# Kernel optimization log

Hardware: AMD Instinct MI355X
Metric: run time of the kernel (lower is better)

## Reference

```python
import jax, jax.numpy as jnp
import numpy as np

BLOCK_LEN = 64

def _segsum(x):
    """x: (..., T) -> (..., T, T) with segment sums on/below diagonal, -inf above."""
    T = x.shape[-1]
    cs = jnp.cumsum(x, axis=-1)
    seg = cs[..., :, None] - cs[..., None, :]
    mask = jnp.tril(jnp.ones((T, T), dtype=bool))
    return jnp.where(mask, seg, -jnp.inf)

def setup_inputs() -> dict:
    key = jax.random.key(0)
    kX, kA, kB, kC = jax.random.split(key, 4)
    B, S, H, P, N = 2, 4096, 32, 64, 64
    X = jax.random.normal(kX, (B, S, H, P), dtype=jnp.float32)
    # negative decay rates keep exp(cumsum) bounded (real Mamba2 uses A<0)
    A = -jnp.abs(jax.random.normal(kA, (B, S, H), dtype=jnp.float32)) * 0.1
    Bm = jax.random.normal(kB, (B, S, H, N), dtype=jnp.float32)
    Cm = jax.random.normal(kC, (B, S, H, N), dtype=jnp.float32)
    return {"X": X, "A": A, "Bm": Bm, "Cm": Cm}

def reference(X, A, Bm, Cm):
    b, s, h, p = X.shape
    n = Bm.shape[-1]
    l = BLOCK_LEN
    c = s // l
    Xb = X.reshape(b, c, l, h, p)
    Bb = Bm.reshape(b, c, l, h, n)
    Cb = Cm.reshape(b, c, l, h, n)
    Ab = A.reshape(b, c, l, h).transpose(0, 3, 1, 2)  # (b,h,c,l)

    # intra-chunk decay matrix L = exp(segsum(A))  (b,h,c,l,l)
    L = jnp.exp(_segsum(Ab))
    Y_diag = jnp.einsum('bclhn,bcshn,bhcls,bcshp->bclhp', Cb, Bb, L, Xb)

    A_cumsum = jnp.cumsum(Ab, axis=-1)  # (b,h,c,l)
    decay_states = jnp.exp(A_cumsum[..., :, -1:] - A_cumsum)
    states = jnp.einsum('bclhn,bhcl,bclhp->bchpn', Bb, decay_states, Xb)

    init = jnp.zeros_like(states[:, :1])
    states = jnp.concatenate([init, states], axis=1)  # (b,c+1,h,p,n)

    chunk_last = jnp.pad(A_cumsum[..., -1], ((0, 0), (0, 0), (1, 0)))  # (b,h,c+1)
    decay_chunk = jnp.exp(_segsum(chunk_last))  # (b,h,c+1,c+1)
    new_states = jnp.einsum('bhzc,bchpn->bzhpn', decay_chunk, states)
    states = new_states[:, :-1]  # (b,c,h,p,n)

    state_decay_out = jnp.exp(A_cumsum)
    Y_off = jnp.einsum('bclhn,bchpn,bhcl->bclhp', Cb, states, state_decay_out)

    Y = (Y_diag + Y_off).reshape(b, s, h, p)
    return Y
```

## Files before the change

kernel.cpp:

```cpp
#include <hip/hip_runtime.h>
#include <hip/hip_bf16.h>

#define B_ 2
#define S_ 4096
#define H_ 32
#define P_ 64
#define N_ 64
#define C_ 64
#define HP 2048
#define HN 2048

__device__ __forceinline__ float bf2f(unsigned int u16) {
    return __uint_as_float(u16 << 16);
}
__device__ __forceinline__ void unpack2(unsigned int u, float& lo, float& hi) {
    lo = __uint_as_float(u << 16);
    hi = __uint_as_float(u & 0xffff0000u);
}
__device__ __forceinline__ unsigned short f2bf(float f) {
    unsigned int u = __float_as_uint(f);
    u += 0x7fffu + ((u >> 16) & 1u);
    return (unsigned short)(u >> 16);
}

__global__ void k0_detect(const unsigned short* __restrict__ Au, int* __restrict__ flag)
{
    int tid = threadIdx.x;
    unsigned short u = Au[tid * 2];
    int positive = ((u & 0x8000u) == 0) ? 1 : 0;
    unsigned long long m = __ballot(positive);
    if (tid == 0) *flag = (__popcll(m) > 8) ? 1 : 0;
}

__global__ __launch_bounds__(256) void k1_states(
    const void* __restrict__ Xg,
    const void* __restrict__ Ag,
    const void* __restrict__ Bg,
    float* __restrict__ states,
    float* __restrict__ sums,
    const int* __restrict__ flag)
{
    __shared__ __align__(16) float Xs[64][68];
    __shared__ __align__(16) float BwT[64][68];
    __shared__ float wdec[64];

    const int tid = threadIdx.x;
    const int bid = blockIdx.x;
    const int h = bid & 31;
    const int c = (bid >> 5) & 63;
    const int b = bid >> 11;
    const int isf32 = *flag;

    if (tid < 64) {
        int ai = (b * S_ + c * 64 + tid) * H_ + h;
        float a = isf32 ? ((const float*)Ag)[ai] : bf2f(((const unsigned short*)Ag)[ai]);
        float x = a;
        #pragma unroll
        for (int off = 1; off < 64; off <<= 1) {
            float y = __shfl_up(x, off, 64);
            if (tid >= off) x += y;
        }
        float tot = __shfl(x, 63, 64);
        wdec[tid] = __expf(tot - x);
        if (tid == 63) sums[(b * H_ + h) * C_ + c] = tot;
    }
    __syncthreads();

    const size_t baseX = (size_t)((b * S_ + c * 64) * H_ + h) * P_;
    const size_t baseB = (size_t)((b * S_ + c * 64) * H_ + h) * N_;

    if (!isf32) {
        const unsigned short* Xp = (const unsigned short*)Xg + baseX;
        const unsigned short* Bp = (const unsigned short*)Bg + baseB;
        #pragma unroll
        for (int it = 0; it < 2; ++it) {
            int f = it * 2048 + tid * 8;
            int t = f >> 6;
            int e = f & 63;
            uint4 rx = *(const uint4*)(Xp + (size_t)t * HP + e);
            float v0,v1,v2,v3,v4,v5,v6,v7;
            unpack2(rx.x, v0, v1); unpack2(rx.y, v2, v3);
            unpack2(rx.z, v4, v5); unpack2(rx.w, v6, v7);
            float* xr = &Xs[t][e];
            xr[0]=v0; xr[1]=v1; xr[2]=v2; xr[3]=v3; xr[4]=v4; xr[5]=v5; xr[6]=v6; xr[7]=v7;

            uint4 rb = *(const uint4*)(Bp + (size_t)t * HN + e);
            float w = wdec[t];
            unpack2(rb.x, v0, v1); unpack2(rb.y, v2, v3);
            unpack2(rb.z, v4, v5); unpack2(rb.w, v6, v7);
            BwT[e+0][t]=v0*w; BwT[e+1][t]=v1*w; BwT[e+2][t]=v2*w; BwT[e+3][t]=v3*w;
            BwT[e+4][t]=v4*w; BwT[e+5][t]=v5*w; BwT[e+6][t]=v6*w; BwT[e+7][t]=v7*w;
        }
    } else {
        const float* Xp = (const float*)Xg + baseX;
        const float* Bp = (const float*)Bg + baseB;
        #pragma unroll
        for (int it = 0; it < 2; ++it) {
            int f = it * 2048 + tid * 8;
            int t = f >> 6;
            int e = f & 63;
            float4 x0 = *(const float4*)(Xp + (size_t)t * HP + e);
            float4 x1 = *(const float4*)(Xp + (size_t)t * HP + e + 4);
            float* xr = &Xs[t][e];
            xr[0]=x0.x; xr[1]=x0.y; xr[2]=x0.z; xr[3]=x0.w;
            xr[4]=x1.x; xr[5]=x1.y; xr[6]=x1.z; xr[7]=x1.w;

            float4 b0 = *(const float4*)(Bp + (size_t)t * HN + e);
            float4 b1 = *(const float4*)(Bp + (size_t)t * HN + e + 4);
            float w = wdec[t];
            BwT[e+0][t]=b0.x*w; BwT[e+1][t]=b0.y*w; BwT[e+2][t]=b0.z*w; BwT[e+3][t]=b0.w*w;
            BwT[e+4][t]=b1.x*w; BwT[e+5][t]=b1.y*w; BwT[e+6][t]=b1.z*w; BwT[e+7][t]=b1.w*w;
        }
    }
    __syncthreads();

    const int tr = tid >> 4, tc = tid & 15;
    float acc[4][4];
    #pragma unroll
    for (int i = 0; i < 4; ++i)
        #pragma unroll
        for (int j = 0; j < 4; ++j) acc[i][j] = 0.f;

    #pragma unroll 4
    for (int k4 = 0; k4 < 16; ++k4) {
        float la[4][4];
        #pragma unroll
        for (int i = 0; i < 4; ++i) {
            float4 v = *(const float4*)&BwT[tr * 4 + i][k4 * 4];
            la[i][0]=v.x; la[i][1]=v.y; la[i][2]=v.z; la[i][3]=v.w;
        }
        #pragma unroll
        for (int kk = 0; kk < 4; ++kk) {
            float4 r = *(const float4*)&Xs[k4 * 4 + kk][tc * 4];
            #pragma unroll
            for (int i = 0; i < 4; ++i) {
                acc[i][0] += la[i][kk] * r.x;
                acc[i][1] += la[i][kk] * r.y;
                acc[i][2] += la[i][kk] * r.z;
                acc[i][3] += la[i][kk] * r.w;
            }
        }
    }

    float* sp = states + (size_t)((b * C_ + c) * H_ + h) * 4096;
    #pragma unroll
    for (int i = 0; i < 4; ++i) {
        float4 v; v.x=acc[i][0]; v.y=acc[i][1]; v.z=acc[i][2]; v.w=acc[i][3];
        *(float4*)&sp[(tr * 4 + i) * 64 + tc * 4] = v;
    }
}

__global__ __launch_bounds__(256) void k2_scan(
    float* __restrict__ states, const float* __restrict__ sums)
{
    const int tid = threadIdx.x;
    const int bid = blockIdx.x;
    const int split = bid & 3;
    const int bh = bid >> 2;
    const int h = bh & 31;
    const int b = bh >> 5;
    const int e = split * 1024 + tid * 4;
    const float* sm = sums + (b * H_ + h) * C_;
    float4 S; S.x=0.f; S.y=0.f; S.z=0.f; S.w=0.f;
    for (int c = 0; c < 64; ++c) {
        float* p = states + (size_t)((b * C_ + c) * H_ + h) * 4096 + e;
        float4 st = *(const float4*)p;
        *(float4*)p = S;
        float d = __expf(sm[c]);
        S.x = S.x * d + st.x;
        S.y = S.y * d + st.y;
        S.z = S.z * d + st.z;
        S.w = S.w * d + st.w;
    }
}

__global__ __launch_bounds__(256) void k3_y(
    const void* __restrict__ Xg,
    const void* __restrict__ Ag,
    const void* __restrict__ Bg,
    const void* __restrict__ Cg,
    const float* __restrict__ states,
    void* __restrict__ Yg,
    const int* __restrict__ flag)
{
    __shared__ __align__(16) float Cs[64][68];
    __shared__ __align__(16) float Mb[64][68];
    __shared__ __align__(16) float Rb[64][68];
    __shared__ float cs[64];

    const int tid = threadIdx.x;
    const int bid = blockIdx.x;
    const int h = bid & 31;
    const int c = (bid >> 5) & 63;
    const int b = bid >> 11;
    const int isf32 = *flag;

    if (tid < 64) {
        int ai = (b * S_ + c * 64 + tid) * H_ + h;
        float a = isf32 ? ((const float*)Ag)[ai] : bf2f(((const unsigned short*)Ag)[ai]);
        float x = a;
        #pragma unroll
        for (int off = 1; off < 64; off <<= 1) {
            float y = __shfl_up(x, off, 64);
            if (tid >= off) x += y;
        }
        cs[tid] = x;
    }

    const size_t baseX = (size_t)((b * S_ + c * 64) * H_ + h) * P_;
    const size_t baseN = (size_t)((b * S_ + c * 64) * H_ + h) * N_;

    if (!isf32) {
        const unsigned short* Bp = (const unsigned short*)Bg + baseN;
        const unsigned short* Cp = (const unsigned short*)Cg + baseN;
        #pragma unroll
        for (int it = 0; it < 2; ++it) {
            int f = it * 2048 + tid * 8;
            int t = f >> 6;
            int e = f & 63;
            uint4 rc = *(const uint4*)(Cp + (size_t)t * HN + e);
            float v0,v1,v2,v3,v4,v5,v6,v7;
            unpack2(rc.x, v0, v1); unpack2(rc.y, v2, v3);
            unpack2(rc.z, v4, v5); unpack2(rc.w, v6, v7);
            float* cr = &Cs[t][e];
            cr[0]=v0; cr[1]=v1; cr[2]=v2; cr[3]=v3; cr[4]=v4; cr[5]=v5; cr[6]=v6; cr[7]=v7;

            uint4 rb = *(const uint4*)(Bp + (size_t)t * HN + e);
            unpack2(rb.x, v0, v1); unpack2(rb.y, v2, v3);
            unpack2(rb.z, v4, v5); unpack2(rb.w, v6, v7);
            Rb[e+0][t]=v0; Rb[e+1][t]=v1; Rb[e+2][t]=v2; Rb[e+3][t]=v3;
            Rb[e+4][t]=v4; Rb[e+5][t]=v5; Rb[e+6][t]=v6; Rb[e+7][t]=v7;
        }
    } else {
        const float* Bp = (const float*)Bg + baseN;
        const float* Cp = (const float*)Cg + baseN;
        #pragma unroll
        for (int it = 0; it < 2; ++it) {
            int f = it * 2048 + tid * 8;
            int t = f >> 6;
            int e = f & 63;
            float4 c0 = *(const float4*)(Cp + (size_t)t * HN + e);
            float4 c1 = *(const float4*)(Cp + (size_t)t * HN + e + 4);
            float* cr = &Cs[t][e];
            cr[0]=c0.x; cr[1]=c0.y; cr[2]=c0.z; cr[3]=c0.w;
            cr[4]=c1.x; cr[5]=c1.y; cr[6]=c1.z; cr[7]=c1.w;

            float4 b0 = *(const float4*)(Bp + (size_t)t * HN + e);
            float4 b1 = *(const float4*)(Bp + (size_t)t * HN + e + 4);
            Rb[e+0][t]=b0.x; Rb[e+1][t]=b0.y; Rb[e+2][t]=b0.z; Rb[e+3][t]=b0.w;
            Rb[e+4][t]=b1.x; Rb[e+5][t]=b1.y; Rb[e+6][t]=b1.z; Rb[e+7][t]=b1.w;
        }
    }
    __syncthreads();

    const int tr = tid >> 4, tc = tid & 15;

    {
        float acc[4][4];
        #pragma unroll
        for (int i = 0; i < 4; ++i)
            #pragma unroll
            for (int j = 0; j < 4; ++j) acc[i][j] = 0.f;

        #pragma unroll 4
        for (int k4 = 0; k4 < 16; ++k4) {
            float la[4][4];
            #pragma unroll
            for (int i = 0; i < 4; ++i) {
                float4 v = *(const float4*)&Cs[tr * 4 + i][k4 * 4];
                la[i][0]=v.x; la[i][1]=v.y; la[i][2]=v.z; la[i][3]=v.w;
            }
            #pragma unroll
            for (int kk = 0; kk < 4; ++kk) {
                float4 r = *(const float4*)&Rb[k4 * 4 + kk][tc * 4];
                #pragma unroll
                for (int i = 0; i < 4; ++i) {
                    acc[i][0] += la[i][kk] * r.x;
                    acc[i][1] += la[i][kk] * r.y;
                    acc[i][2] += la[i][kk] * r.z;
                    acc[i][3] += la[i][kk] * r.w;
                }
            }
        }

        float ct[4], csj[4];
        #pragma unroll
        for (int i = 0; i < 4; ++i) ct[i] = cs[tr * 4 + i];
        #pragma unroll
        for (int j = 0; j < 4; ++j) csj[j] = cs[tc * 4 + j];
        #pragma unroll
        for (int i = 0; i < 4; ++i) {
            int t = tr * 4 + i;
            float4 mv;
            mv.x = (tc*4+0 <= t) ? acc[i][0] * __expf(ct[i]-csj[0]) : 0.f;
            mv.y = (tc*4+1 <= t) ? acc[i][1] * __expf(ct[i]-csj[1]) : 0.f;
            mv.z = (tc*4+2 <= t) ? acc[i][2] * __expf(ct[i]-csj[2]) : 0.f;
            mv.w = (tc*4+3 <= t) ? acc[i][3] * __expf(ct[i]-csj[3]) : 0.f;
            *(float4*)&Mb[t][tc * 4] = mv;
        }
    }
    __syncthreads();

    if (!isf32) {
        const unsigned short* Xp = (const unsigned short*)Xg + baseX;
        #pragma unroll
        for (int it = 0; it < 2; ++it) {
            int f = it * 2048 + tid * 8;
            int t = f >> 6;
            int e = f & 63;
            uint4 rx = *(const uint4*)(Xp + (size_t)t * HP + e);
            float v0,v1,v2,v3,v4,v5,v6,v7;
            unpack2(rx.x, v0, v1); unpack2(rx.y, v2, v3);
            unpack2(rx.z, v4, v5); unpack2(rx.w, v6, v7);
            float* xr = &Rb[t][e];
            xr[0]=v0; xr[1]=v1; xr[2]=v2; xr[3]=v3; xr[4]=v4; xr[5]=v5; xr[6]=v6; xr[7]=v7;
        }
    } else {
        const float* Xp = (const float*)Xg + baseX;
        #pragma unroll
        for (int it = 0; it < 2; ++it) {
            int f = it * 2048 + tid * 8;
            int t = f >> 6;
            int e = f & 63;
            float4 x0 = *(const float4*)(Xp + (size_t)t * HP + e);
            float4 x1 = *(const float4*)(Xp + (size_t)t * HP + e + 4);
            float* xr = &Rb[t][e];
            xr[0]=x0.x; xr[1]=x0.y; xr[2]=x0.z; xr[3]=x0.w;
            xr[4]=x1.x; xr[5]=x1.y; xr[6]=x1.z; xr[7]=x1.w;
        }
    }
    __syncthreads();

    float accD[4][4];
    #pragma unroll
    for (int i = 0; i < 4; ++i)
        #pragma unroll
        for (int j = 0; j < 4; ++j) accD[i][j] = 0.f;

    #pragma unroll 4
    for (int k4 = 0; k4 < 16; ++k4) {
        float la[4][4];
        #pragma unroll
        for (int i = 0; i < 4; ++i) {
            float4 v = *(const float4*)&Mb[tr * 4 + i][k4 * 4];
            la[i][0]=v.x; la[i][1]=v.y; la[i][2]=v.z; la[i][3]=v.w;
        }
        #pragma unroll
        for (int kk = 0; kk < 4; ++kk) {
            float4 r = *(const float4*)&Rb[k4 * 4 + kk][tc * 4];
            #pragma unroll
            for (int i = 0; i < 4; ++i) {
                accD[i][0] += la[i][kk] * r.x;
                accD[i][1] += la[i][kk] * r.y;
                accD[i][2] += la[i][kk] * r.z;
                accD[i][3] += la[i][kk] * r.w;
            }
        }
    }
    __syncthreads();

    {
        const float* sb = states + (size_t)((b * C_ + c) * H_ + h) * 4096;
        #pragma unroll
        for (int k = 0; k < 4; ++k) {
            int e2 = (k * 256 + tid) * 4;
            float4 v = *(const float4*)(sb + e2);
            *(float4*)&Rb[e2 >> 6][e2 & 63] = v;
        }
    }
    __syncthreads();

    float accO[4][4];
    #pragma unroll
    for (int i = 0; i < 4; ++i)
        #pragma unroll
        for (int j = 0; j < 4; ++j) accO[i][j] = 0.f;

    #pragma unroll 4
    for (int k4 = 0; k4 < 16; ++k4) {
        float la[4][4];
        #pragma unroll
        for (int i = 0; i < 4; ++i) {
            float4 v = *(const float4*)&Cs[tr * 4 + i][k4 * 4];
            la[i][0]=v.x; la[i][1]=v.y; la[i][2]=v.z; la[i][3]=v.w;
        }
        #pragma unroll
        for (int kk = 0; kk < 4; ++kk) {
            float4 r = *(const float4*)&Rb[k4 * 4 + kk][tc * 4];
            #pragma unroll
            for (int i = 0; i < 4; ++i) {
                accO[i][0] += la[i][kk] * r.x;
                accO[i][1] += la[i][kk] * r.y;
                accO[i][2] += la[i][kk] * r.z;
                accO[i][3] += la[i][kk] * r.w;
            }
        }
    }

    if (!isf32) {
        unsigned short* Yp = (unsigned short*)Yg + baseX;
        #pragma unroll
        for (int i = 0; i < 4; ++i) {
            int t = tr * 4 + i;
            float g = __expf(cs[t]);
            ushort4 o;
            o.x = f2bf(accD[i][0] + g * accO[i][0]);
            o.y = f2bf(accD[i][1] + g * accO[i][1]);
            o.z = f2bf(accD[i][2] + g * accO[i][2]);
            o.w = f2bf(accD[i][3] + g * accO[i][3]);
            *(ushort4*)(Yp + (size_t)t * HP + tc * 4) = o;
        }
    } else {
        float* Yp = (float*)Yg + baseX;
        #pragma unroll
        for (int i = 0; i < 4; ++i) {
            int t = tr * 4 + i;
            float g = __expf(cs[t]);
            float4 o;
            o.x = accD[i][0] + g * accO[i][0];
            o.y = accD[i][1] + g * accO[i][1];
            o.z = accD[i][2] + g * accO[i][2];
            o.w = accD[i][3] + g * accO[i][3];
            *(float4*)(Yp + (size_t)t * HP + tc * 4) = o;
        }
    }
}

extern "C" void kernel_launch(void* const* d_in, const int* in_sizes, int n_in,
                              void* d_out, int out_size, void* d_ws, size_t ws_size,
                              hipStream_t stream) {
    const void* X  = d_in[0];
    const void* A  = d_in[1];
    const void* Bm = d_in[2];
    const void* Cm = d_in[3];

    int*   flag   = (int*)d_ws;
    float* sums   = (float*)d_ws + 16;
    float* states = (float*)d_ws + 16 + 4096;

    k0_detect<<<dim3(1), dim3(64), 0, stream>>>((const unsigned short*)A, flag);
    k1_states<<<dim3(B_ * C_ * H_), dim3(256), 0, stream>>>(X, A, Bm, states, sums, flag);
    k2_scan  <<<dim3(B_ * H_ * 4),  dim3(256), 0, stream>>>(states, sums);
    k3_y     <<<dim3(B_ * C_ * H_), dim3(256), 0, stream>>>(X, A, Bm, Cm, states, d_out, flag);
}
```

Baseline: 334.1 us.

## Use split-bf16 MFMA matmuls in state and output kernels, widen scan split

Replaces the scalar FP32 shared-memory GEMMs in the chunk-state and output kernels with bf16 MFMA 16x16x32 instructions. Each fp32 operand is split into high and low bf16 parts and combined with three products, which keeps close to fp32 accuracy. Shared tiles move to swizzled bf16 layouts to avoid bank conflicts, and launch bounds are set to raise occupancy. The scan kernel is split eight ways with float2 accesses and a prefetch of the next chunk. The cost is extra split/convert work, more shared memory, and scalar (non-vector) global stores of the MFMA output layout.

Measured after the change: 282.6 us. -15.4%, faster.

```diff
diff --git a/kernel.cpp b/kernel.cpp
--- a/kernel.cpp
+++ b/kernel.cpp
@@ -1,5 +1,4 @@
 #include <hip/hip_runtime.h>
-#include <hip/hip_bf16.h>
 
 #define B_ 2
 #define S_ 4096
@@ -10,6 +9,9 @@
 #define HP 2048
 #define HN 2048
 
+typedef __attribute__((ext_vector_type(8))) short bf16x8;
+typedef __attribute__((ext_vector_type(4))) float f32x4;
+
 __device__ __forceinline__ float bf2f(unsigned int u16) {
     return __uint_as_float(u16 << 16);
 }
@@ -21,6 +23,17 @@
     unsigned int u = __float_as_uint(f);
     u += 0x7fffu + ((u >> 16) & 1u);
     return (unsigned short)(u >> 16);
+}
+__device__ __forceinline__ void split_bf(float x, unsigned short& h, unsigned short& l) {
+    h = f2bf(x);
+    l = f2bf(x - bf2f(h));
+}
+
+__device__ __forceinline__ int nsw(int r, int cb) {
+    return (r << 7) + (cb ^ ((r & 7) << 4));
+}
+__device__ __forceinline__ int tsw(int r, int cb) {
+    return (r << 7) + (cb ^ ((((r & 7) ^ (r >> 3)) & 7) << 4));
 }
 
 __global__ void k0_detect(const unsigned short* __restrict__ Au, int* __restrict__ flag)
@@ -32,7 +45,7 @@
     if (tid == 0) *flag = (__popcll(m) > 8) ? 1 : 0;
 }
 
-__global__ __launch_bounds__(256) void k1_states(
+__global__ __launch_bounds__(256, 4) void k1u(
     const void* __restrict__ Xg,
     const void* __restrict__ Ag,
     const void* __restrict__ Bg,
@@ -40,15 +53,15 @@
     float* __restrict__ sums,
     const int* __restrict__ flag)
 {
-    __shared__ __align__(16) float Xs[64][68];
-    __shared__ __align__(16) float BwT[64][68];
+    __shared__ __align__(16) unsigned short XTh[4096];
+    __shared__ __align__(16) unsigned short XTl[4096];
+    __shared__ __align__(16) unsigned short BTh[4096];
+    __shared__ __align__(16) unsigned short BTl[4096];
     __shared__ float wdec[64];
 
     const int tid = threadIdx.x;
     const int bid = blockIdx.x;
-    const int h = bid & 31;
-    const int c = (bid >> 5) & 63;
-    const int b = bid >> 11;
+    const int h = bid & 31, c = (bid >> 5) & 63, b = bid >> 11;
     const int isf32 = *flag;
 
     if (tid < 64) {
@@ -68,86 +81,91 @@
 
     const size_t baseX = (size_t)((b * S_ + c * 64) * H_ + h) * P_;
     const size_t baseB = (size_t)((b * S_ + c * 64) * H_ + h) * N_;
-
-    if (!isf32) {
-        const unsigned short* Xp = (const unsigned short*)Xg + baseX;
-        const unsigned short* Bp = (const unsigned short*)Bg + baseB;
-        #pragma unroll
-        for (int it = 0; it < 2; ++it) {
-            int f = it * 2048 + tid * 8;
-            int t = f >> 6;
-            int e = f & 63;
-            uint4 rx = *(const uint4*)(Xp + (size_t)t * HP + e);
-            float v0,v1,v2,v3,v4,v5,v6,v7;
-            unpack2(rx.x, v0, v1); unpack2(rx.y, v2, v3);
-            unpack2(rx.z, v4, v5); unpack2(rx.w, v6, v7);
-            float* xr = &Xs[t][e];
-            xr[0]=v0; xr[1]=v1; xr[2]=v2; xr[3]=v3; xr[4]=v4; xr[5]=v5; xr[6]=v6; xr[7]=v7;
-
-            uint4 rb = *(const uint4*)(Bp + (size_t)t * HN + e);
-            float w = wdec[t];
-            unpack2(rb.x, v0, v1); unpack2(rb.y, v2, v3);
-            unpack2(rb.z, v4, v5); unpack2(rb.w, v6, v7);
-            BwT[e+0][t]=v0*w; BwT[e+1][t]=v1*w; BwT[e+2][t]=v2*w; BwT[e+3][t]=v3*w;
-            BwT[e+4][t]=v4*w; BwT[e+5][t]=v5*w; BwT[e+6][t]=v6*w; BwT[e+7][t]=v7*w;
-        }
-    } else {
-        const float* Xp = (const float*)Xg + baseX;
-        const float* Bp = (const float*)Bg + baseB;
-        #pragma unroll
-        for (int it = 0; it < 2; ++it) {
-            int f = it * 2048 + tid * 8;
-            int t = f >> 6;
-            int e = f & 63;
-            float4 x0 = *(const float4*)(Xp + (size_t)t * HP + e);
-            float4 x1 = *(const float4*)(Xp + (size_t)t * HP + e + 4);
-            float* xr = &Xs[t][e];
-            xr[0]=x0.x; xr[1]=x0.y; xr[2]=x0.z; xr[3]=x0.w;
-            xr[4]=x1.x; xr[5]=x1.y; xr[6]=x1.z; xr[7]=x1.w;
-
-            float4 b0 = *(const float4*)(Bp + (size_t)t * HN + e);
-            float4 b1 = *(const float4*)(Bp + (size_t)t * HN + e + 4);
-            float w = wdec[t];
-            BwT[e+0][t]=b0.x*w; BwT[e+1][t]=b0.y*w; BwT[e+2][t]=b0.z*w; BwT[e+3][t]=b0.w*w;
-            BwT[e+4][t]=b1.x*w; BwT[e+5][t]=b1.y*w; BwT[e+6][t]=b1.z*w; BwT[e+7][t]=b1.w*w;
+    char* XThb = (char*)XTh;
+    char* XTlb = (char*)XTl;
+    char* BThb = (char*)BTh;
+    char* BTlb = (char*)BTl;
+
+    #pragma unroll
+    for (int it = 0; it < 2; ++it) {
+        int t = (tid >> 3) + it * 32;
+        int e = (tid & 7) * 8;
+        float xv[8], bv[8];
+        if (isf32) {
+            const float* Xp = (const float*)Xg + baseX + (size_t)t * HP + e;
+            const float* Bp = (const float*)Bg + baseB + (size_t)t * HN + e;
+            float4 x0 = *(const float4*)Xp;
+            float4 x1 = *(const float4*)(Xp + 4);
+            float4 b0 = *(const float4*)Bp;
+            float4 b1 = *(const float4*)(Bp + 4);
+            xv[0]=x0.x; xv[1]=x0.y; xv[2]=x0.z; xv[3]=x0.w;
+            xv[4]=x1.x; xv[5]=x1.y; xv[6]=x1.z; xv[7]=x1.w;
+            bv[0]=b0.x; bv[1]=b0.y; bv[2]=b0.z; bv[3]=b0.w;
+            bv[4]=b1.x; bv[5]=b1.y; bv[6]=b1.z; bv[7]=b1.w;
+        } else {
+            const unsigned short* Xp = (const unsigned short*)Xg + baseX + (size_t)t * HP + e;
+            const unsigned short* Bp = (const unsigned short*)Bg + baseB + (size_t)t * HN + e;
+            uint4 rx = *(const uint4*)Xp;
+            uint4 rb = *(const uint4*)Bp;
+            unpack2(rx.x, xv[0], xv[1]); unpack2(rx.y, xv[2], xv[3]);
+            unpack2(rx.z, xv[4], xv[5]); unpack2(rx.w, xv[6], xv[7]);
+            unpack2(rb.x, bv[0], bv[1]); unpack2(rb.y, bv[2], bv[3]);
+            unpack2(rb.z, bv[4], bv[5]); unpack2(rb.w, bv[6], bv[7]);
+        }
+        float w = wdec[t];
+        #pragma unroll
+        for (int i = 0; i < 8; ++i) {
+            int o = tsw(e + i, 2 * t);
+            unsigned short hh, ll;
+            split_bf(xv[i], hh, ll);
+            *(unsigned short*)(XThb + o) = hh;
+            *(unsigned short*)(XTlb + o) = ll;
+            split_bf(bv[i] * w, hh, ll);
+            *(unsigned short*)(BThb + o) = hh;
+            *(unsigned short*)(BTlb + o) = ll;
         }
     }
     __syncthreads();
 
-    const int tr = tid >> 4, tc = tid & 15;
-    float acc[4][4];
-    #pragma unroll
-    for (int i = 0; i < 4; ++i)
-        #pragma unroll
-        for (int j = 0; j < 4; ++j) acc[i][j] = 0.f;
-
-    #pragma unroll 4
-    for (int k4 = 0; k4 < 16; ++k4) {
-        float la[4][4];
-        #pragma unroll
-        for (int i = 0; i < 4; ++i) {
-            float4 v = *(const float4*)&BwT[tr * 4 + i][k4 * 4];
-            la[i][0]=v.x; la[i][1]=v.y; la[i][2]=v.z; la[i][3]=v.w;
-        }
-        #pragma unroll
-        for (int kk = 0; kk < 4; ++kk) {
-            float4 r = *(const float4*)&Xs[k4 * 4 + kk][tc * 4];
-            #pragma unroll
-            for (int i = 0; i < 4; ++i) {
-                acc[i][0] += la[i][kk] * r.x;
-                acc[i][1] += la[i][kk] * r.y;
-                acc[i][2] += la[i][kk] * r.z;
-                acc[i][3] += la[i][kk] * r.w;
-            }
-        }
+    const int l = tid & 63, w4 = tid >> 6;
+    const int lr = l & 15, q = l >> 4;
+    const int rowA = 16 * w4 + lr;
+
+    const int oa0 = tsw(rowA, 16 * q);
+    const int oa1 = tsw(rowA, 16 * q + 64);
+    bf16x8 a0h = *(const bf16x8*)(XThb + oa0);
+    bf16x8 a1h = *(const bf16x8*)(XThb + oa1);
+    bf16x8 a0l = *(const bf16x8*)(XTlb + oa0);
+    bf16x8 a1l = *(const bf16x8*)(XTlb + oa1);
+
+    f32x4 acc[4];
+    #pragma unroll
+    for (int nt = 0; nt < 4; ++nt) acc[nt] = (f32x4){0.f, 0.f, 0.f, 0.f};
+    #pragma unroll
+    for (int nt = 0; nt < 4; ++nt) {
+        int ob0 = tsw(16 * nt + lr, 16 * q);
+        int ob1 = tsw(16 * nt + lr, 16 * q + 64);
+        bf16x8 b0h = *(const bf16x8*)(BThb + ob0);
+        bf16x8 b0l = *(const bf16x8*)(BTlb + ob0);
+        bf16x8 b1h = *(const bf16x8*)(BThb + ob1);
+        bf16x8 b1l = *(const bf16x8*)(BTlb + ob1);
+        acc[nt] = __builtin_amdgcn_mfma_f32_16x16x32_bf16(a0h, b0h, acc[nt], 0, 0, 0);
+        acc[nt] = __builtin_amdgcn_mfma_f32_16x16x32_bf16(a1h, b1h, acc[nt], 0, 0, 0);
+        acc[nt] = __builtin_amdgcn_mfma_f32_16x16x32_bf16(a0h, b0l, acc[nt], 0, 0, 0);
+        acc[nt] = __builtin_amdgcn_mfma_f32_16x16x32_bf16(a1h, b1l, acc[nt], 0, 0, 0);
+        acc[nt] = __builtin_amdgcn_mfma_f32_16x16x32_bf16(a0l, b0h, acc[nt], 0, 0, 0);
+        acc[nt] = __builtin_amdgcn_mfma_f32_16x16x32_bf16(a1l, b1h, acc[nt], 0, 0, 0);
     }
 
     float* sp = states + (size_t)((b * C_ + c) * H_ + h) * 4096;
     #pragma unroll
-    for (int i = 0; i < 4; ++i) {
-        float4 v; v.x=acc[i][0]; v.y=acc[i][1]; v.z=acc[i][2]; v.w=acc[i][3];
-        *(float4*)&sp[(tr * 4 + i) * 64 + tc * 4] = v;
-    }
+    for (int nt = 0; nt < 4; ++nt)
+        #pragma unroll
+        for (int r = 0; r < 4; ++r) {
+            int p = 16 * w4 + 4 * q + r;
+            int n = 16 * nt + lr;
+            sp[p * 64 + n] = acc[nt][r];
+        }
 }
 
 __global__ __launch_bounds__(256) void k2_scan(
@@ -155,26 +173,30 @@
 {
     const int tid = threadIdx.x;
     const int bid = blockIdx.x;
-    const int split = bid & 3;
-    const int bh = bid >> 2;
+    const int split = bid & 7;
+    const int bh = bid >> 3;
     const int h = bh & 31;
     const int b = bh >> 5;
-    const int e = split * 1024 + tid * 4;
+    const int e = split * 512 + tid * 2;
     const float* sm = sums + (b * H_ + h) * C_;
-    float4 S; S.x=0.f; S.y=0.f; S.z=0.f; S.w=0.f;
+    const size_t cstride = (size_t)H_ * 4096;
+    float* p = states + ((size_t)(b * C_) * H_ + h) * 4096 + e;
+    float2 S = make_float2(0.f, 0.f);
+    float2 st = *(const float2*)p;
+    #pragma unroll 4
     for (int c = 0; c < 64; ++c) {
-        float* p = states + (size_t)((b * C_ + c) * H_ + h) * 4096 + e;
-        float4 st = *(const float4*)p;
-        *(float4*)p = S;
+        float2 stn = make_float2(0.f, 0.f);
+        if (c < 63) stn = *(const float2*)(p + cstride);
         float d = __expf(sm[c]);
+        *(float2*)p = S;
         S.x = S.x * d + st.x;
         S.y = S.y * d + st.y;
-        S.z = S.z * d + st.z;
-        S.w = S.w * d + st.w;
-    }
-}
-
-__global__ __launch_bounds__(256) void k3_y(
+        st = stn;
+        p += cstride;
+    }
+}
+
+__global__ __launch_bounds__(256, 3) void k3u(
     const void* __restrict__ Xg,
     const void* __restrict__ Ag,
     const void* __restrict__ Bg,
@@ -183,16 +205,17 @@
     void* __restrict__ Yg,
     const int* __restrict__ flag)
 {
-    __shared__ __align__(16) float Cs[64][68];
-    __shared__ __align__(16) float Mb[64][68];
-    __shared__ __align__(16) float Rb[64][68];
-    __shared__ float cs[64];
+    __shared__ __align__(16) unsigned short Ch[4096];
+    __shared__ __align__(16) unsigned short Cl[4096];
+    __shared__ __align__(16) unsigned short Bh[4096];
+    __shared__ __align__(16) unsigned short Bl[4096];
+    __shared__ __align__(16) unsigned short Sh[4096];
+    __shared__ __align__(16) unsigned short Sl[4096];
+    __shared__ float csh[64];
 
     const int tid = threadIdx.x;
     const int bid = blockIdx.x;
-    const int h = bid & 31;
-    const int c = (bid >> 5) & 63;
-    const int b = bid >> 11;
+    const int h = bid & 31, c = (bid >> 5) & 63, b = bid >> 11;
     const int isf32 = *flag;
 
     if (tid < 64) {
@@ -204,160 +227,89 @@
             float y = __shfl_up(x, off, 64);
             if (tid >= off) x += y;
         }
-        cs[tid] = x;
+        csh[tid] = x;
     }
 
     const size_t baseX = (size_t)((b * S_ + c * 64) * H_ + h) * P_;
     const size_t baseN = (size_t)((b * S_ + c * 64) * H_ + h) * N_;
-
-    if (!isf32) {
-        const unsigned short* Bp = (const unsigned short*)Bg + baseN;
-        const unsigned short* Cp = (const unsigned short*)Cg + baseN;
-        #pragma unroll
-        for (int it = 0; it < 2; ++it) {
-            int f = it * 2048 + tid * 8;
-            int t = f >> 6;
-            int e = f & 63;
-            uint4 rc = *(const uint4*)(Cp + (size_t)t * HN + e);
-            float v0,v1,v2,v3,v4,v5,v6,v7;
-            unpack2(rc.x, v0, v1); unpack2(rc.y, v2, v3);
-            unpack2(rc.z, v4, v5); unpack2(rc.w, v6, v7);
-            float* cr = &Cs[t][e];
-            cr[0]=v0; cr[1]=v1; cr[2]=v2; cr[3]=v3; cr[4]=v4; cr[5]=v5; cr[6]=v6; cr[7]=v7;
-
-            uint4 rb = *(const uint4*)(Bp + (size_t)t * HN + e);
-            unpack2(rb.x, v0, v1); unpack2(rb.y, v2, v3);
-            unpack2(rb.z, v4, v5); unpack2(rb.w, v6, v7);
-            Rb[e+0][t]=v0; Rb[e+1][t]=v1; Rb[e+2][t]=v2; Rb[e+3][t]=v3;
-            Rb[e+4][t]=v4; Rb[e+5][t]=v5; Rb[e+6][t]=v6; Rb[e+7][t]=v7;
-        }
-    } else {
-        const float* Bp = (const float*)Bg + baseN;
-        const float* Cp = (const float*)Cg + baseN;
-        #pragma unroll
-        for (int it = 0; it < 2; ++it) {
-            int f = it * 2048 + tid * 8;
-            int t = f >> 6;
-            int e = f & 63;
-            float4 c0 = *(const float4*)(Cp + (size_t)t * HN + e);
-            float4 c1 = *(const float4*)(Cp + (size_t)t * HN + e + 4);
-            float* cr = &Cs[t][e];
-            cr[0]=c0.x; cr[1]=c0.y; cr[2]=c0.z; cr[3]=c0.w;
-            cr[4]=c1.x; cr[5]=c1.y; cr[6]=c1.z; cr[7]=c1.w;
-
-            float4 b0 = *(const float4*)(Bp + (size_t)t * HN + e);
-            float4 b1 = *(const float4*)(Bp + (size_t)t * HN + e + 4);
-            Rb[e+0][t]=b0.x; Rb[e+1][t]=b0.y; Rb[e+2][t]=b0.z; Rb[e+3][t]=b0.w;
-            Rb[e+4][t]=b1.x; Rb[e+5][t]=b1.y; Rb[e+6][t]=b1.z; Rb[e+7][t]=b1.w;
-        }
-    }
-    __syncthreads();
-
-    const int tr = tid >> 4, tc = tid & 15;
-
-    {
-        float acc[4][4];
-        #pragma unroll
-        for (int i = 0; i < 4; ++i)
-            #pragma unroll
-            for (int j = 0; j < 4; ++j) acc[i][j] = 0.f;
-
-        #pragma unroll 4
-        for (int k4 = 0; k4 < 16; ++k4) {
-            float la[4][4];
-            #pragma unroll
-            for (int i = 0; i < 4; ++i) {
-                float4 v = *(const float4*)&Cs[tr * 4 + i][k4 * 4];
-                la[i][0]=v.x; la[i][1]=v.y; la[i][2]=v.z; la[i][3]=v.w;
-            }
-            #pragma unroll
-            for (int kk = 0; kk < 4; ++kk) {
-                float4 r = *(const float4*)&Rb[k4 * 4 + kk][tc * 4];
-                #pragma unroll
-                for (int i = 0; i < 4; ++i) {
-                    acc[i][0] += la[i][kk] * r.x;
-                    acc[i][1] += la[i][kk] * r.y;
-                    acc[i][2] += la[i][kk] * r.z;
-                    acc[i][3] += la[i][kk] * r.w;
-                }
-            }
-        }
-
-        float ct[4], csj[4];
-        #pragma unroll
-        for (int i = 0; i < 4; ++i) ct[i] = cs[tr * 4 + i];
-        #pragma unroll
-        for (int j = 0; j < 4; ++j) csj[j] = cs[tc * 4 + j];
-        #pragma unroll
-        for (int i = 0; i < 4; ++i) {
-            int t = tr * 4 + i;
-            float4 mv;
-            mv.x = (tc*4+0 <= t) ? acc[i][0] * __expf(ct[i]-csj[0]) : 0.f;
-            mv.y = (tc*4+1 <= t) ? acc[i][1] * __expf(ct[i]-csj[1]) : 0.f;
-            mv.z = (tc*4+2 <= t) ? acc[i][2] * __expf(ct[i]-csj[2]) : 0.f;
-            mv.w = (tc*4+3 <= t) ? acc[i][3] * __expf(ct[i]-csj[3]) : 0.f;
-            *(float4*)&Mb[t][tc * 4] = mv;
-        }
-    }
-    __syncthreads();
-
-    if (!isf32) {
-        const unsigned short* Xp = (const unsigned short*)Xg + baseX;
-        #pragma unroll
-        for (int it = 0; it < 2; ++it) {
-            int f = it * 2048 + tid * 8;
-            int t = f >> 6;
-            int e = f & 63;
-            uint4 rx = *(const uint4*)(Xp + (size_t)t * HP + e);
-            float v0,v1,v2,v3,v4,v5,v6,v7;
-            unpack2(rx.x, v0, v1); unpack2(rx.y, v2, v3);
-            unpack2(rx.z, v4, v5); unpack2(rx.w, v6, v7);
-            float* xr = &Rb[t][e];
-            xr[0]=v0; xr[1]=v1; xr[2]=v2; xr[3]=v3; xr[4]=v4; xr[5]=v5; xr[6]=v6; xr[7]=v7;
-        }
-    } else {
-        const float* Xp = (const float*)Xg + baseX;
-        #pragma unroll
-        for (int it = 0; it < 2; ++it) {
-            int f = it * 2048 + tid * 8;
-            int t = f >> 6;
-            int e = f & 63;
-            float4 x0 = *(const float4*)(Xp + (size_t)t * HP + e);
-            float4 x1 = *(const float4*)(Xp + (size_t)t * HP + e + 4);
-            float* xr = &Rb[t][e];
-            xr[0]=x0.x; xr[1]=x0.y; xr[2]=x0.z; xr[3]=x0.w;
-            xr[4]=x1.x; xr[5]=x1.y; xr[6]=x1.z; xr[7]=x1.w;
-        }
-    }
-    __syncthreads();
-
-    float accD[4][4];
-    #pragma unroll
-    for (int i = 0; i < 4; ++i)
-        #pragma unroll
-        for (int j = 0; j < 4; ++j) accD[i][j] = 0.f;
-
-    #pragma unroll 4
-    for (int k4 = 0; k4 < 16; ++k4) {
-        float la[4][4];
-        #pragma unroll
-        for (int i = 0; i < 4; ++i) {
-            float4 v = *(const float4*)&Mb[tr * 4 + i][k4 * 4];
-            la[i][0]=v.x; la[i][1]=v.y; la[i][2]=v.z; la[i][3]=v.w;
-        }
-        #pragma unroll
-        for (int kk = 0; kk < 4; ++kk) {
-            float4 r = *(const float4*)&Rb[k4 * 4 + kk][tc * 4];
-            #pragma unroll
-            for (int i = 0; i < 4; ++i) {
-                accD[i][0] += la[i][kk] * r.x;
-                accD[i][1] += la[i][kk] * r.y;
-                accD[i][2] += la[i][kk] * r.z;
-                accD[i][3] += la[i][kk] * r.w;
-            }
-        }
-    }
-    __syncthreads();
+    char* Chb = (char*)Ch; char* Clb = (char*)Cl;
+    char* Bhb = (char*)Bh; char* Blb = (char*)Bl;
+    char* Shb = (char*)Sh; char* Slb = (char*)Sl;
+
+    uint4 xq0[2], xq1[2];
+    #pragma unroll
+    for (int it = 0; it < 2; ++it) {
+        int t = (tid >> 3) + it * 32;
+        int e = (tid & 7) * 8;
+        if (isf32) {
+            const float* Xp = (const float*)Xg + baseX + (size_t)t * HP + e;
+            xq0[it] = *(const uint4*)Xp;
+            xq1[it] = *(const uint4*)(Xp + 4);
+        } else {
+            const unsigned short* Xp = (const unsigned short*)Xg + baseX + (size_t)t * HP + e;
+            xq0[it] = *(const uint4*)Xp;
+        }
+    }
+
+    #pragma unroll
+    for (int it = 0; it < 2; ++it) {
+        int t = (tid >> 3) + it * 32;
+        int e = (tid & 7) * 8;
+        float cv[8], bv[8];
+        if (isf32) {
+            const float* Cp = (const float*)Cg + baseN + (size_t)t * HN + e;
+            const float* Bp = (const float*)Bg + baseN + (size_t)t * HN + e;
+            float4 c0 = *(const float4*)Cp;
+            float4 c1 = *(const float4*)(Cp + 4);
+            float4 b0 = *(const float4*)Bp;
+            float4 b1 = *(const float4*)(Bp + 4);
+            cv[0]=c0.x; cv[1]=c0.y; cv[2]=c0.z; cv[3]=c0.w;
+            cv[4]=c1.x; cv[5]=c1.y; cv[6]=c1.z; cv[7]=c1.w;
+            bv[0]=b0.x; bv[1]=b0.y; bv[2]=b0.z; bv[3]=b0.w;
+            bv[4]=b1.x; bv[5]=b1.y; bv[6]=b1.z; bv[7]=b1.w;
+        } else {
+            const unsigned short* Cp = (const unsigned short*)Cg + baseN + (size_t)t * HN + e;
+            const unsigned short* Bp = (const unsigned short*)Bg + baseN + (size_t)t * HN + e;
+            uint4 rc = *(const uint4*)Cp;
+            uint4 rb = *(const uint4*)Bp;
+            unpack2(rc.x, cv[0], cv[1]); unpack2(rc.y, cv[2], cv[3]);
+            unpack2(rc.z, cv[4], cv[5]); unpack2(rc.w, cv[6], cv[7]);
+            unpack2(rb.x, bv[0], bv[1]); unpack2(rb.y, bv[2], bv[3]);
+            unpack2(rb.z, bv[4], bv[5]); unpack2(rb.w, bv[6], bv[7]);
+        }
+        int o = nsw(t, 2 * e);
+        unsigned short hs[8], ls[8];
+        #pragma unroll
+        for (int i = 0; i < 8; ++i) split_bf(cv[i], hs[i], ls[i]);
+        {
+            uint4 uh, ul;
+            uh.x = (unsigned int)hs[0] | ((unsigned int)hs[1] << 16);
+            uh.y = (unsigned int)hs[2] | ((unsigned int)hs[3] << 16);
+            uh.z = (unsigned int)hs[4] | ((unsigned int)hs[5] << 16);
+            uh.w = (unsigned int)hs[6] | ((unsigned int)hs[7] << 16);
+            ul.x = (unsigned int)ls[0] | ((unsigned int)ls[1] << 16);
+            ul.y = (unsigned int)ls[2] | ((unsigned int)ls[3] << 16);
+            ul.z = (unsigned int)ls[4] | ((unsigned int)ls[5] << 16);
+            ul.w = (unsigned int)ls[6] | ((unsigned int)ls[7] << 16);
+            *(uint4*)(Chb + o) = uh;
+            *(uint4*)(Clb + o) = ul;
+        }
+        #pragma unroll
+        for (int i = 0; i < 8; ++i) split_bf(bv[i], hs[i], ls[i]);
+        {
+            uint4 uh, ul;
+            uh.x = (unsigned int)hs[0] | ((unsigned int)hs[1] << 16);
+            uh.y = (unsigned int)hs[2] | ((unsigned int)hs[3] << 16);
+            uh.z = (unsigned int)hs[4] | ((unsigned int)hs[5] << 16);
+            uh.w = (unsigned int)hs[6] | ((unsigned int)hs[7] << 16);
+            ul.x = (unsigned int)ls[0] | ((unsigned int)ls[1] << 16);
+            ul.y = (unsigned int)ls[2] | ((unsigned int)ls[3] << 16);
+            ul.z = (unsigned int)ls[4] | ((unsigned int)ls[5] << 16);
+            ul.w = (unsigned int)ls[6] | ((unsigned int)ls[7] << 16);
+            *(uint4*)(Bhb + o) = uh;
+            *(uint4*)(Blb + o) = ul;
+        }
+    }
 
     {
         const float* sb = states + (size_t)((b * C_ + c) * H_ + h) * 4096;
@@ -365,64 +317,161 @@
         for (int k = 0; k < 4; ++k) {
             int e2 = (k * 256 + tid) * 4;
             float4 v = *(const float4*)(sb + e2);
-            *(float4*)&Rb[e2 >> 6][e2 & 63] = v;
+            unsigned short h0,l0,h1,l1,h2,l2,h3,l3;
+            split_bf(v.x, h0, l0); split_bf(v.y, h1, l1);
+            split_bf(v.z, h2, l2); split_bf(v.w, h3, l3);
+            uint2 uh, ul;
+            uh.x = (unsigned int)h0 | ((unsigned int)h1 << 16);
+            uh.y = (unsigned int)h2 | ((unsigned int)h3 << 16);
+            ul.x = (unsigned int)l0 | ((unsigned int)l1 << 16);
+            ul.y = (unsigned int)l2 | ((unsigned int)l3 << 16);
+            int o = nsw(e2 >> 6, 2 * (e2 & 63));
+            *(uint2*)(Shb + o) = uh;
+            *(uint2*)(Slb + o) = ul;
         }
     }
     __syncthreads();
 
-    float accO[4][4];
-    #pragma unroll
-    for (int i = 0; i < 4; ++i)
-        #pragma unroll
-        for (int j = 0; j < 4; ++j) accO[i][j] = 0.f;
-
-    #pragma unroll 4
-    for (int k4 = 0; k4 < 16; ++k4) {
-        float la[4][4];
-        #pragma unroll
-        for (int i = 0; i < 4; ++i) {
-            float4 v = *(const float4*)&Cs[tr * 4 + i][k4 * 4];
-            la[i][0]=v.x; la[i][1]=v.y; la[i][2]=v.z; la[i][3]=v.w;
-        }
-        #pragma unroll
-        for (int kk = 0; kk < 4; ++kk) {
-            float4 r = *(const float4*)&Rb[k4 * 4 + kk][tc * 4];
-            #pragma unroll
-            for (int i = 0; i < 4; ++i) {
-                accO[i][0] += la[i][kk] * r.x;
-                accO[i][1] += la[i][kk] * r.y;
-                accO[i][2] += la[i][kk] * r.z;
-                accO[i][3] += la[i][kk] * r.w;
-            }
-        }
-    }
-
+    const int l = tid & 63, w4 = tid >> 6;
+    const int lr = l & 15, q = l >> 4;
+    const int tA = 16 * w4 + lr;
+
+    const int oa0 = nsw(tA, 16 * q);
+    const int oa1 = nsw(tA, 16 * q + 64);
+    bf16x8 ac0h = *(const bf16x8*)(Chb + oa0);
+    bf16x8 ac1h = *(const bf16x8*)(Chb + oa1);
+    bf16x8 ac0l = *(const bf16x8*)(Clb + oa0);
+    bf16x8 ac1l = *(const bf16x8*)(Clb + oa1);
+
+    f32x4 mac[4];
+    #pragma unroll
+    for (int st = 0; st < 4; ++st) mac[st] = (f32x4){0.f, 0.f, 0.f, 0.f};
+    #pragma unroll
+    for (int st = 0; st < 4; ++st) {
+        int ob0 = nsw(16 * st + lr, 16 * q);
+        int ob1 = nsw(16 * st + lr, 16 * q + 64);
+        bf16x8 b0h = *(const bf16x8*)(Bhb + ob0);
+        bf16x8 b0l = *(const bf16x8*)(Blb + ob0);
+        bf16x8 b1h = *(const bf16x8*)(Bhb + ob1);
+        bf16x8 b1l = *(const bf16x8*)(Blb + ob1);
+        mac[st] = __builtin_amdgcn_mfma_f32_16x16x32_bf16(ac0h, b0h, mac[st], 0, 0, 0);
+        mac[st] = __builtin_amdgcn_mfma_f32_16x16x32_bf16(ac1h, b1h, mac[st], 0, 0, 0);
+        mac[st] = __builtin_amdgcn_mfma_f32_16x16x32_bf16(ac0h, b0l, mac[st], 0, 0, 0);
+        mac[st] = __builtin_amdgcn_mfma_f32_16x16x32_bf16(ac1h, b1l, mac[st], 0, 0, 0);
+        mac[st] = __builtin_amdgcn_mfma_f32_16x16x32_bf16(ac0l, b0h, mac[st], 0, 0, 0);
+        mac[st] = __builtin_amdgcn_mfma_f32_16x16x32_bf16(ac1l, b1h, mac[st], 0, 0, 0);
+    }
+
+    f32x4 yacO[4];
+    #pragma unroll
+    for (int pt = 0; pt < 4; ++pt) yacO[pt] = (f32x4){0.f, 0.f, 0.f, 0.f};
+    #pragma unroll
+    for (int pt = 0; pt < 4; ++pt) {
+        int os0 = nsw(16 * pt + lr, 16 * q);
+        int os1 = nsw(16 * pt + lr, 16 * q + 64);
+        bf16x8 s0h = *(const bf16x8*)(Shb + os0);
+        bf16x8 s0l = *(const bf16x8*)(Slb + os0);
+        bf16x8 s1h = *(const bf16x8*)(Shb + os1);
+        bf16x8 s1l = *(const bf16x8*)(Slb + os1);
+        yacO[pt] = __builtin_amdgcn_mfma_f32_16x16x32_bf16(ac0h, s0h, yacO[pt], 0, 0, 0);
+        yacO[pt] = __builtin_amdgcn_mfma_f32_16x16x32_bf16(ac1h, s1h, yacO[pt], 0, 0, 0);
+        yacO[pt] = __builtin_amdgcn_mfma_f32_16x16x32_bf16(ac0h, s0l, yacO[pt], 0, 0, 0);
+        yacO[pt] = __builtin_amdgcn_mfma_f32_16x16x32_bf16(ac1h, s1l, yacO[pt], 0, 0, 0);
+        yacO[pt] = __builtin_amdgcn_mfma_f32_16x16x32_bf16(ac0l, s0h, yacO[pt], 0, 0, 0);
+        yacO[pt] = __builtin_amdgcn_mfma_f32_16x16x32_bf16(ac1l, s1h, yacO[pt], 0, 0, 0);
+    }
+    __syncthreads();
+
+    float ct[4];
+    #pragma unroll
+    for (int r = 0; r < 4; ++r) ct[r] = csh[16 * w4 + 4 * q + r];
+    #pragma unroll
+    for (int st = 0; st < 4; ++st) {
+        int s = 16 * st + lr;
+        float cs_s = csh[s];
+        #pragma unroll
+        for (int r = 0; r < 4; ++r) {
+            int t = 16 * w4 + 4 * q + r;
+            float v = (s <= t) ? mac[st][r] * __expf(ct[r] - cs_s) : 0.f;
+            unsigned short hh, ll;
+            split_bf(v, hh, ll);
+            int o = nsw(t, 2 * s);
+            *(unsigned short*)(Bhb + o) = hh;
+            *(unsigned short*)(Blb + o) = ll;
+        }
+    }
+
+    #pragma unroll
+    for (int it = 0; it < 2; ++it) {
+        int t = (tid >> 3) + it * 32;
+        int e = (tid & 7) * 8;
+        float xv[8];
+        if (isf32) {
+            xv[0] = __uint_as_float(xq0[it].x); xv[1] = __uint_as_float(xq0[it].y);
+            xv[2] = __uint_as_float(xq0[it].z); xv[3] = __uint_as_float(xq0[it].w);
+            xv[4] = __uint_as_float(xq1[it].x); xv[5] = __uint_as_float(xq1[it].y);
+            xv[6] = __uint_as_float(xq1[it].z); xv[7] = __uint_as_float(xq1[it].w);
+        } else {
+            unpack2(xq0[it].x, xv[0], xv[1]); unpack2(xq0[it].y, xv[2], xv[3]);
+            unpack2(xq0[it].z, xv[4], xv[5]); unpack2(xq0[it].w, xv[6], xv[7]);
+        }
+        #pragma unroll
+        for (int i = 0; i < 8; ++i) {
+            unsigned short hh, ll;
+            split_bf(xv[i], hh, ll);
+            int o = tsw(e + i, 2 * t);
+            *(unsigned short*)(Shb + o) = hh;
+            *(unsigned short*)(Slb + o) = ll;
+        }
+    }
+    __syncthreads();
+
+    const int om0 = nsw(tA, 16 * q);
+    const int om1 = nsw(tA, 16 * q + 64);
+    bf16x8 am0h = *(const bf16x8*)(Bhb + om0);
+    bf16x8 am1h = *(const bf16x8*)(Bhb + om1);
+    bf16x8 am0l = *(const bf16x8*)(Blb + om0);
+    bf16x8 am1l = *(const bf16x8*)(Blb + om1);
+    f32x4 yacD[4];
+    #pragma unroll
+    for (int pt = 0; pt < 4; ++pt) yacD[pt] = (f32x4){0.f, 0.f, 0.f, 0.f};
+    #pragma unroll
+    for (int pt = 0; pt < 4; ++pt) {
+        int ox0 = tsw(16 * pt + lr, 16 * q);
+        int ox1 = tsw(16 * pt + lr, 16 * q + 64);
+        bf16x8 x0h = *(const bf16x8*)(Shb + ox0);
+        bf16x8 x0l = *(const bf16x8*)(Slb + ox0);
+        bf16x8 x1h = *(const bf16x8*)(Shb + ox1);
+        bf16x8 x1l = *(const bf16x8*)(Slb + ox1);
+        yacD[pt] = __builtin_amdgcn_mfma_f32_16x16x32_bf16(am0h, x0h, yacD[pt], 0, 0, 0);
+        yacD[pt] = __builtin_amdgcn_mfma_f32_16x16x32_bf16(am1h, x1h, yacD[pt], 0, 0, 0);
+        yacD[pt] = __builtin_amdgcn_mfma_f32_16x16x32_bf16(am0h, x0l, yacD[pt], 0, 0, 0);
+        yacD[pt] = __builtin_amdgcn_mfma_f32_16x16x32_bf16(am1h, x1l, yacD[pt], 0, 0, 0);
+        yacD[pt] = __builtin_amdgcn_mfma_f32_16x16x32_bf16(am0l, x0h, yacD[pt], 0, 0, 0);
+        yacD[pt] = __builtin_amdgcn_mfma_f32_16x16x32_bf16(am1l, x1h, yacD[pt], 0, 0, 0);
+    }
+
+    float ge[4];
+    #pragma unroll
+    for (int r = 0; r < 4; ++r) ge[r] = __expf(ct[r]);
     if (!isf32) {
         unsigned short* Yp = (unsigned short*)Yg + baseX;
         #pragma unroll
-        for (int i = 0; i < 4; ++i) {
-            int t = tr * 4 + i;
-            float g = __expf(cs[t]);
-            ushort4 o;
-            o.x = f2bf(accD[i][0] + g * accO[i][0]);
-            o.y = f2bf(accD[i][1] + g * accO[i][1]);
-            o.z = f2bf(accD[i][2] + g * accO[i][2]);
-            o.w = f2bf(accD[i][3] + g * accO[i][3]);
-            *(ushort4*)(Yp + (size_t)t * HP + tc * 4) = o;
-        }
+        for (int pt = 0; pt < 4; ++pt)
+            #pragma unroll
+            for (int r = 0; r < 4; ++r) {
+                int t = 16 * w4 + 4 * q + r;
+                Yp[(size_t)t * HP + 16 * pt + lr] = f2bf(yacD[pt][r] + ge[r] * yacO[pt][r]);
+            }
     } else {
         float* Yp = (float*)Yg + baseX;
         #pragma unroll
-        for (int i = 0; i < 4; ++i) {
-            int t = tr * 4 + i;
-            float g = __expf(cs[t]);
-            float4 o;
-            o.x = accD[i][0] + g * accO[i][0];
-            o.y = accD[i][1] + g * accO[i][1];
-            o.z = accD[i][2] + g * accO[i][2];
-            o.w = accD[i][3] + g * accO[i][3];
-            *(float4*)(Yp + (size_t)t * HP + tc * 4) = o;
-        }
+        for (int pt = 0; pt < 4; ++pt)
+            #pragma unroll
+            for (int r = 0; r < 4; ++r) {
+                int t = 16 * w4 + 4 * q + r;
+                Yp[(size_t)t * HP + 16 * pt + lr] = yacD[pt][r] + ge[r] * yacO[pt][r];
+            }
     }
 }
 
@@ -439,7 +488,7 @@
     float* states = (float*)d_ws + 16 + 4096;
 
     k0_detect<<<dim3(1), dim3(64), 0, stream>>>((const unsigned short*)A, flag);
-    k1_states<<<dim3(B_ * C_ * H_), dim3(256), 0, stream>>>(X, A, Bm, states, sums, flag);
-    k2_scan  <<<dim3(B_ * H_ * 4),  dim3(256), 0, stream>>>(states, sums);
-    k3_y     <<<dim3(B_ * C_ * H_), dim3(256), 0, stream>>>(X, A, Bm, Cm, states, d_out, flag);
-}
+    k1u<<<dim3(B_ * C_ * H_), dim3(256), 0, stream>>>(X, A, Bm, states, sums, flag);
+    k2_scan<<<dim3(B_ * H_ * 8), dim3(256), 0, stream>>>(states, sums);
+    k3u<<<dim3(B_ * C_ * H_), dim3(256), 0, stream>>>(X, A, Bm, Cm, states, d_out, flag);
+}
```
